# Kernel optimization log

Hardware: AMD Instinct MI355X
Metric: run time of the kernel (lower is better)

The kernel has to match this reference:

```python
import jax, jax.numpy as jnp
import numpy as np

DIM = 1024

def setup_inputs() -> dict:
    key = jax.random.key(0)
    ks = jax.random.split(key, 7)
    s = 1.0 / np.sqrt(DIM)  # roughly match nn.Linear init scale
    return {
        "x": jax.random.normal(ks[0], (4, 2048, DIM), dtype=jnp.float32),
        "Wq": jax.random.normal(ks[1], (DIM, DIM), dtype=jnp.float32) * s,
        "bq": jax.random.normal(ks[2], (DIM,), dtype=jnp.float32) * s,
        "Wk": jax.random.normal(ks[3], (DIM, DIM), dtype=jnp.float32) * s,
        "bk": jax.random.normal(ks[4], (DIM,), dtype=jnp.float32) * s,
        "Wv": jax.random.normal(ks[5], (DIM, DIM), dtype=jnp.float32) * s,
        "bv": jax.random.normal(ks[6], (DIM,), dtype=jnp.float32) * s,
    }

def reference(x, Wq, bq, Wk, bk, Wv, bv):
    # torch Linear: y = x @ W.T + b
    C = x.shape[-1]
    scale = C ** (-0.5)
    q = jnp.einsum('bnc,dc->bnd', x, Wq) + bq
    k = jnp.einsum('bnc,dc->bnd', x, Wk) + bk
    v = jnp.einsum('bnc,dc->bnd', x, Wv) + bv
    attn = jnp.einsum('bnd,bmd->bnm', q, k) * scale  # [B,N,N]
    attn = jax.nn.softmax(attn, axis=-1)
    out = jnp.einsum('bnm,bmd->bnd', attn, v)
    return out
```

## Files before the change

kernel.cpp:

```cpp
#include <hip/hip_runtime.h>

#define SEQ  2048
#define DIM  1024
#define NTOK 8192
#define NQKV 3072

typedef __attribute__((ext_vector_type(8))) __bf16 bf16x8;
typedef __attribute__((ext_vector_type(4))) float  f32x4;

__device__ __forceinline__ unsigned short f2bf(float f) {
    unsigned int u = __float_as_uint(f);
    u += 0x7fffu + ((u >> 16) & 1u);
    return (unsigned short)(u >> 16);
}

__device__ __forceinline__ float bfu2f(unsigned int lo16) {
    return __uint_as_float(lo16 << 16);
}

__device__ __forceinline__ void load_lds_128(const unsigned short* g, unsigned short* l) {
    __builtin_amdgcn_global_load_lds(
        (const __attribute__((address_space(1))) void*)g,
        (__attribute__((address_space(3))) void*)l, 16, 0, 0);
}

#define BAR() asm volatile("s_barrier" ::: "memory")

#define CLUSTER(AFR, NB, MBASE)                                            \
    do {                                                                   \
        __builtin_amdgcn_s_setprio(1);                                     \
        _Pragma("unroll")                                                  \
        for (int mf = 0; mf < 4; ++mf)                                     \
            _Pragma("unroll")                                              \
            for (int nn = 0; nn < 2; ++nn)                                 \
                _Pragma("unroll")                                          \
                for (int kk = 0; kk < 2; ++kk)                             \
                    acc[(MBASE) + mf][(NB) + nn] =                         \
                        __builtin_amdgcn_mfma_f32_16x16x32_bf16(           \
                            AFR[mf][kk], bfr[(NB) + nn][kk],               \
                            acc[(MBASE) + mf][(NB) + nn], 0, 0, 0);        \
        __builtin_amdgcn_s_setprio(0);                                     \
    } while (0)

template <int MODE, int MB>
__global__ __launch_bounds__(512, 2)
void gemm2(const unsigned short* __restrict__ A, const unsigned short* __restrict__ B,
           void* __restrict__ Cv,
           const float* __restrict__ b0v, const float* __restrict__ b1v,
           const float* __restrict__ b2v, unsigned short* __restrict__ vt,
           const float* __restrict__ inv_rs,
           int K, int lda, int ldb, int ldc,
           long sA, long sB, long sC, float alpha)
{
    constexpr int BM = MB * 128;
    constexpr int AT = BM * 64;
    constexpr int BT = 256 * 64;
    __shared__ __align__(16) unsigned short As[2 * AT];
    __shared__ __align__(16) unsigned short Bs[2 * BT];

    const int tid  = threadIdx.x;
    const int wave = tid >> 6;
    const int lane = tid & 63;
    const int l4   = lane & 15;
    const int lh   = lane >> 4;
    const int wm   = wave >> 2;
    const int wn   = wave & 3;

    const int m0 = blockIdx.x * BM;
    const int n0 = blockIdx.y * 256;
    const int z  = blockIdx.z;
    A += (long)z * sA;
    B += (long)z * sB;

    const int r0 = tid >> 3;
    const int gc = (tid & 7) ^ (r0 & 7);
    const unsigned short* Ag = A + (long)(m0 + r0) * lda + gc * 8;
    const unsigned short* Bg = B + (long)(n0 + r0) * ldb + gc * 8;
    unsigned short* Al = As + tid * 8;
    unsigned short* Bl = Bs + tid * 8;

    const int NT = K >> 6;

    auto stage = [&](int t, int u) {
        const long kof = (long)t * 64;
#pragma unroll
        for (int p = 0; p < 2 * MB; ++p)
            load_lds_128(Ag + kof + (long)(64 * p) * lda, Al + u * AT + p * 4096);
#pragma unroll
        for (int p = 0; p < 4; ++p)
            load_lds_128(Bg + kof + (long)(64 * p) * ldb, Bl + u * BT + p * 4096);
    };

    const int aoff = (wm * (BM / 2) + l4) * 64;
    const int boff = (wn * 64 + l4) * 64;
    const int cs0  = ((0 + lh) ^ (lane & 7)) * 8;
    const int cs1  = ((4 + lh) ^ (lane & 7)) * 8;

    f32x4 acc[4 * MB][4] = {};
    bf16x8 bfr[4][2], alo[4][2], ahi[4][2];

    stage(0, 0);
    asm volatile("s_waitcnt vmcnt(0)" ::: "memory");
    BAR();

    for (int t = 0; t < NT; ++t) {
        const int u = t & 1;
        const unsigned short* Ab = As + u * AT + aoff;
        const unsigned short* Bb = Bs + u * BT + boff;

#pragma unroll
        for (int nn = 0; nn < 2; ++nn) {
            bfr[nn][0] = *(const bf16x8*)(Bb + nn * 1024 + cs0);
            bfr[nn][1] = *(const bf16x8*)(Bb + nn * 1024 + cs1);
        }
#pragma unroll
        for (int mf = 0; mf < 4; ++mf) {
            alo[mf][0] = *(const bf16x8*)(Ab + mf * 1024 + cs0);
            alo[mf][1] = *(const bf16x8*)(Ab + mf * 1024 + cs1);
        }
#pragma unroll
        for (int nn = 2; nn < 4; ++nn) {
            bfr[nn][0] = *(const bf16x8*)(Bb + nn * 1024 + cs0);
            bfr[nn][1] = *(const bf16x8*)(Bb + nn * 1024 + cs1);
        }
        if (t + 1 < NT) stage(t + 1, u ^ 1);

        if constexpr (MB == 2) {
            CLUSTER(alo, 0, 0);
#pragma unroll
            for (int mf = 0; mf < 4; ++mf) {
                ahi[mf][0] = *(const bf16x8*)(Ab + (4 + mf) * 1024 + cs0);
                ahi[mf][1] = *(const bf16x8*)(Ab + (4 + mf) * 1024 + cs1);
            }
            CLUSTER(alo, 2, 0);
            CLUSTER(ahi, 2, 4);
            asm volatile("s_waitcnt vmcnt(0) lgkmcnt(0)" ::: "memory");
            BAR();
            CLUSTER(ahi, 0, 4);
        } else {
            CLUSTER(alo, 0, 0);
            asm volatile("s_waitcnt vmcnt(0) lgkmcnt(0)" ::: "memory");
            BAR();
            CLUSTER(alo, 2, 0);
        }
    }

    const int r0c = m0 + wm * (BM / 2) + lh * 4;
    const int c0c = n0 + wn * 64 + l4;

    if (MODE == 0) {
        if (n0 >= 2048) {
#pragma unroll
            for (int nf = 0; nf < 4; ++nf) {
                const int d = c0c + nf * 16 - 2048;
                const float bias = b2v[d];
#pragma unroll
                for (int mf = 0; mf < 4 * MB; ++mf) {
                    const int row = r0c + mf * 16;
                    const int bb = row >> 11;
                    const int mm = row & 2047;
                    ushort4 u;
                    u.x = f2bf(acc[mf][nf][0] + bias);
                    u.y = f2bf(acc[mf][nf][1] + bias);
                    u.z = f2bf(acc[mf][nf][2] + bias);
                    u.w = f2bf(acc[mf][nf][3] + bias);
                    *(ushort4*)(vt + ((long)bb * DIM + d) * SEQ + mm) = u;
                }
            }
        } else {
            unsigned short* C16 = (unsigned short*)Cv;
#pragma unroll
            for (int nf = 0; nf < 4; ++nf) {
                const int col = c0c + nf * 16;
                const float bias = (col >= 1024) ? b1v[col - 1024] : b0v[col];
#pragma unroll
                for (int mf = 0; mf < 4 * MB; ++mf)
#pragma unroll
                    for (int r = 0; r < 4; ++r)
                        C16[(long)(r0c + mf * 16 + r) * ldc + col] =
                            f2bf(acc[mf][nf][r] + bias);
            }
        }
    } else if (MODE == 1) {
        float* C = (float*)Cv + (long)z * sC;
        const float* ir = inv_rs + (long)z * SEQ;
#pragma unroll
        for (int mf = 0; mf < 4 * MB; ++mf) {
            const int row = r0c + mf * 16;
            const float4 inv4 = *(const float4*)(ir + row);
#pragma unroll
            for (int nf = 0; nf < 4; ++nf) {
                const int col = c0c + nf * 16;
                C[(long)(row + 0) * ldc + col] = acc[mf][nf][0] * inv4.x;
                C[(long)(row + 1) * ldc + col] = acc[mf][nf][1] * inv4.y;
                C[(long)(row + 2) * ldc + col] = acc[mf][nf][2] * inv4.z;
                C[(long)(row + 3) * ldc + col] = acc[mf][nf][3] * inv4.w;
            }
        }
    } else {
        unsigned short* C16 = (unsigned short*)Cv + (long)z * sC;
#pragma unroll
        for (int nf = 0; nf < 4; ++nf) {
            const int col = c0c + nf * 16;
#pragma unroll
            for (int mf = 0; mf < 4 * MB; ++mf)
#pragma unroll
                for (int r = 0; r < 4; ++r)
                    C16[(long)(r0c + mf * 16 + r) * ldc + col] =
                        f2bf(__expf(acc[mf][nf][r] * alpha));
        }
    }
}

__global__ __launch_bounds__(256)
void cvt_x(const float* __restrict__ src, unsigned short* __restrict__ dst, int n4)
{
    int i = blockIdx.x * 256 + threadIdx.x;
    if (i < n4) {
        float4 f = ((const float4*)src)[i];
        ushort4 u;
        u.x = f2bf(f.x); u.y = f2bf(f.y); u.z = f2bf(f.z); u.w = f2bf(f.w);
        ((ushort4*)dst)[i] = u;
    }
}

__global__ __launch_bounds__(256)
void cvt_w3(const float* __restrict__ Wq, const float* __restrict__ Wk,
            const float* __restrict__ Wv, unsigned short* __restrict__ dst)
{
    const int sel = blockIdx.y;
    const float* src = (sel == 0) ? Wq : ((sel == 1) ? Wk : Wv);
    const int i = blockIdx.x * 256 + threadIdx.x;
    float4 f = ((const float4*)src)[i];
    ushort4 u;
    u.x = f2bf(f.x); u.y = f2bf(f.y); u.z = f2bf(f.z); u.w = f2bf(f.w);
    ((ushort4*)(dst + (long)sel * DIM * DIM))[i] = u;
}

__global__ __launch_bounds__(256)
void rowsum_inv(const unsigned short* __restrict__ P, float* __restrict__ inv_rs)
{
    const int row  = blockIdx.x * 4 + (threadIdx.x >> 6);
    const int lane = threadIdx.x & 63;
    const unsigned short* pr = P + (long)row * SEQ;

    float s = 0.f;
#pragma unroll
    for (int it = 0; it < 4; ++it) {
        uint4 u = *(const uint4*)(pr + (it * 64 + lane) * 8);
        s += bfu2f(u.x & 0xffffu) + __uint_as_float(u.x & 0xffff0000u);
        s += bfu2f(u.y & 0xffffu) + __uint_as_float(u.y & 0xffff0000u);
        s += bfu2f(u.z & 0xffffu) + __uint_as_float(u.z & 0xffff0000u);
        s += bfu2f(u.w & 0xffffu) + __uint_as_float(u.w & 0xffff0000u);
    }
    for (int off = 32; off > 0; off >>= 1)
        s += __shfl_xor(s, off);
    if (lane == 0) inv_rs[row] = 1.0f / s;
}

extern "C" void kernel_launch(void* const* d_in, const int* in_sizes, int n_in,
                              void* d_out, int out_size, void* d_ws, size_t ws_size,
                              hipStream_t stream)
{
    const float* x  = (const float*)d_in[0];
    const float* Wq = (const float*)d_in[1];
    const float* bq = (const float*)d_in[2];
    const float* Wk = (const float*)d_in[3];
    const float* bk = (const float*)d_in[4];
    const float* Wv = (const float*)d_in[5];
    const float* bv = (const float*)d_in[6];
    float* out = (float*)d_out;

    char* ws = (char*)d_ws;
    unsigned short* xb   = (unsigned short*)ws;
    unsigned short* Wb   = (unsigned short*)(ws + 16u * 1024 * 1024);
    unsigned short* qkv  = (unsigned short*)(ws + 64u * 1024 * 1024);
    unsigned short* vt   = (unsigned short*)(ws + 112u * 1024 * 1024);
    unsigned short* P    = (unsigned short*)(ws + 128u * 1024 * 1024);
    float*          irs  = (float*)(ws + 160u * 1024 * 1024);

    const float scale = 0.03125f;
    dim3 blk(256);
    dim3 blk512(512);

    cvt_x<<<NTOK * DIM / 4 / 256, blk, 0, stream>>>(x, xb, NTOK * DIM / 4);
    cvt_w3<<<dim3(DIM * DIM / 4 / 256, 3), blk, 0, stream>>>(Wq, Wk, Wv, Wb);

    gemm2<0, 1><<<dim3(NTOK / 128, NQKV / 256), blk512, 0, stream>>>(
        xb, Wb, qkv, bq, bk, bv, vt, nullptr,
        DIM, DIM, DIM, NQKV, 0, 0, 0, 1.0f);

    gemm2<2, 2><<<dim3(SEQ / 256, SEQ / 256, 4), blk512, 0, stream>>>(
        qkv, qkv + 1024, P, nullptr, nullptr, nullptr, nullptr, nullptr,
        DIM, NQKV, NQKV, SEQ,
        (long)SEQ * NQKV, (long)SEQ * NQKV, (long)SEQ * SEQ, scale);

    rowsum_inv<<<NTOK / 4, blk, 0, stream>>>(P, irs);

    gemm2<1, 1><<<dim3(SEQ / 128, DIM / 256, 4), blk512, 0, stream>>>(
        P, vt, out, nullptr, nullptr, nullptr, nullptr, irs,
        SEQ, SEQ, SEQ, DIM,
        (long)SEQ * SEQ, (long)DIM * SEQ, (long)SEQ * DIM, 1.0f);
}
```

Measured before the change: 252.1 us.

## Split GEMM into QK and MN kernels with finer-grained staged LDS pipelining

Replaces the templated gemm2 with two kernels. gemm_qk keeps a 256x256 tile but splits each K-step into four quadrant phases, interleaving half-tile global-to-LDS prefetches with MFMA clusters under partial vmcnt waits. gemm_mn uses 256x128 tiles with a two-phase schedule for the QKV projection and the PV product. The intent is to overlap global loads, LDS reads and MFMA issue more tightly, at the cost of more barriers per K-step and a new tile shape for the projection and output GEMMs.

```diff
diff --git a/kernel.cpp b/kernel.cpp
--- a/kernel.cpp
+++ b/kernel.cpp
@@ -24,36 +24,36 @@
         (__attribute__((address_space(3))) void*)l, 16, 0, 0);
 }
 
-#define BAR() asm volatile("s_barrier" ::: "memory")
-
-#define CLUSTER(AFR, NB, MBASE)                                            \
+#define BAR()   asm volatile("s_barrier" ::: "memory")
+#define LGKM0() do { asm volatile("s_waitcnt lgkmcnt(0)" ::: "memory"); \
+                     __builtin_amdgcn_sched_barrier(0); } while (0)
+#define VMCNT(pf, N)                                                       \
+    do { if (pf) asm volatile("s_waitcnt vmcnt(" #N ")" ::: "memory");     \
+         else    asm volatile("s_waitcnt vmcnt(0)" ::: "memory"); } while (0)
+
+
+#define CLUS_QK(MH, NH)                                                    \
     do {                                                                   \
         __builtin_amdgcn_s_setprio(1);                                     \
         _Pragma("unroll")                                                  \
-        for (int mf = 0; mf < 4; ++mf)                                     \
+        for (int m = 0; m < 4; ++m)                                        \
             _Pragma("unroll")                                              \
-            for (int nn = 0; nn < 2; ++nn)                                 \
-                _Pragma("unroll")                                          \
-                for (int kk = 0; kk < 2; ++kk)                             \
-                    acc[(MBASE) + mf][(NB) + nn] =                         \
-                        __builtin_amdgcn_mfma_f32_16x16x32_bf16(           \
-                            AFR[mf][kk], bfr[(NB) + nn][kk],               \
-                            acc[(MBASE) + mf][(NB) + nn], 0, 0, 0);        \
+            for (int n = 0; n < 2; ++n) {                                  \
+                acc[MH][m][NH][n] = __builtin_amdgcn_mfma_f32_16x16x32_bf16( \
+                    aR[m][0], bR[n][0], acc[MH][m][NH][n], 0, 0, 0);       \
+                acc[MH][m][NH][n] = __builtin_amdgcn_mfma_f32_16x16x32_bf16( \
+                    aR[m][1], bR[n][1], acc[MH][m][NH][n], 0, 0, 0);       \
+            }                                                              \
         __builtin_amdgcn_s_setprio(0);                                     \
     } while (0)
 
-template <int MODE, int MB>
 __global__ __launch_bounds__(512, 2)
-void gemm2(const unsigned short* __restrict__ A, const unsigned short* __restrict__ B,
-           void* __restrict__ Cv,
-           const float* __restrict__ b0v, const float* __restrict__ b1v,
-           const float* __restrict__ b2v, unsigned short* __restrict__ vt,
-           const float* __restrict__ inv_rs,
-           int K, int lda, int ldb, int ldc,
-           long sA, long sB, long sC, float alpha)
-{
-    constexpr int BM = MB * 128;
-    constexpr int AT = BM * 64;
+void gemm_qk(const unsigned short* __restrict__ A, const unsigned short* __restrict__ B,
+             unsigned short* __restrict__ C,
+             int K, int lda, int ldb, int ldc,
+             long sA, long sB, long sC, float alpha)
+{
+    constexpr int AT = 256 * 64;
     constexpr int BT = 256 * 64;
     __shared__ __align__(16) unsigned short As[2 * AT];
     __shared__ __align__(16) unsigned short Bs[2 * BT];
@@ -66,7 +66,7 @@
     const int wm   = wave >> 2;
     const int wn   = wave & 3;
 
-    const int m0 = blockIdx.x * BM;
+    const int m0 = blockIdx.x * 256;
     const int n0 = blockIdx.y * 256;
     const int z  = blockIdx.z;
     A += (long)z * sA;
@@ -81,134 +81,261 @@
 
     const int NT = K >> 6;
 
-    auto stage = [&](int t, int u) {
+    auto stA = [&](int t, int u, int half) {
         const long kof = (long)t * 64;
-#pragma unroll
-        for (int p = 0; p < 2 * MB; ++p)
-            load_lds_128(Ag + kof + (long)(64 * p) * lda, Al + u * AT + p * 4096);
-#pragma unroll
-        for (int p = 0; p < 4; ++p)
-            load_lds_128(Bg + kof + (long)(64 * p) * ldb, Bl + u * BT + p * 4096);
-    };
-
-    const int aoff = (wm * (BM / 2) + l4) * 64;
-    const int boff = (wn * 64 + l4) * 64;
-    const int cs0  = ((0 + lh) ^ (lane & 7)) * 8;
+        load_lds_128(Ag + kof + (long)(64 * (2 * half + 0)) * lda, Al + u * AT + (2 * half + 0) * 4096);
+        load_lds_128(Ag + kof + (long)(64 * (2 * half + 1)) * lda, Al + u * AT + (2 * half + 1) * 4096);
+    };
+    auto stB = [&](int t, int u, int half) {
+        const long kof = (long)t * 64;
+        load_lds_128(Bg + kof + (long)(64 * (2 * half + 0)) * ldb, Bl + u * BT + (2 * half + 0) * 4096);
+        load_lds_128(Bg + kof + (long)(64 * (2 * half + 1)) * ldb, Bl + u * BT + (2 * half + 1) * 4096);
+    };
+
+    const int aoff = (wm * 64 + l4) * 64;
+    const int boff = (wn * 32 + l4) * 64;
+    const int cs0  = (lh ^ (lane & 7)) * 8;
     const int cs1  = ((4 + lh) ^ (lane & 7)) * 8;
 
-    f32x4 acc[4 * MB][4] = {};
-    bf16x8 bfr[4][2], alo[4][2], ahi[4][2];
-
-    stage(0, 0);
-    asm volatile("s_waitcnt vmcnt(0)" ::: "memory");
+    f32x4 acc[2][4][2][2] = {};
+    bf16x8 aR[4][2], bR[2][2];
+
+    auto rdA = [&](const unsigned short* Ab, int mh) {
+#pragma unroll
+        for (int m = 0; m < 4; ++m) {
+            aR[m][0] = *(const bf16x8*)(Ab + mh * 8192 + m * 1024 + cs0);
+            aR[m][1] = *(const bf16x8*)(Ab + mh * 8192 + m * 1024 + cs1);
+        }
+    };
+    auto rdB = [&](const unsigned short* Bb, int nh) {
+#pragma unroll
+        for (int n = 0; n < 2; ++n) {
+            bR[n][0] = *(const bf16x8*)(Bb + nh * 8192 + n * 1024 + cs0);
+            bR[n][1] = *(const bf16x8*)(Bb + nh * 8192 + n * 1024 + cs1);
+        }
+    };
+
+    stA(0, 0, 0); stB(0, 0, 0); stB(0, 0, 1); stA(0, 0, 1);
+    asm volatile("s_waitcnt vmcnt(4)" ::: "memory");
     BAR();
 
     for (int t = 0; t < NT; ++t) {
-        const int u = t & 1;
+        const int u  = t & 1;
+        const int pf = (t + 1 < NT);
         const unsigned short* Ab = As + u * AT + aoff;
         const unsigned short* Bb = Bs + u * BT + boff;
 
-#pragma unroll
-        for (int nn = 0; nn < 2; ++nn) {
-            bfr[nn][0] = *(const bf16x8*)(Bb + nn * 1024 + cs0);
-            bfr[nn][1] = *(const bf16x8*)(Bb + nn * 1024 + cs1);
-        }
-#pragma unroll
-        for (int mf = 0; mf < 4; ++mf) {
-            alo[mf][0] = *(const bf16x8*)(Ab + mf * 1024 + cs0);
-            alo[mf][1] = *(const bf16x8*)(Ab + mf * 1024 + cs1);
-        }
-#pragma unroll
-        for (int nn = 2; nn < 4; ++nn) {
-            bfr[nn][0] = *(const bf16x8*)(Bb + nn * 1024 + cs0);
-            bfr[nn][1] = *(const bf16x8*)(Bb + nn * 1024 + cs1);
-        }
-        if (t + 1 < NT) stage(t + 1, u ^ 1);
-
-        if constexpr (MB == 2) {
-            CLUSTER(alo, 0, 0);
-#pragma unroll
-            for (int mf = 0; mf < 4; ++mf) {
-                ahi[mf][0] = *(const bf16x8*)(Ab + (4 + mf) * 1024 + cs0);
-                ahi[mf][1] = *(const bf16x8*)(Ab + (4 + mf) * 1024 + cs1);
-            }
-            CLUSTER(alo, 2, 0);
-            CLUSTER(ahi, 2, 4);
-            asm volatile("s_waitcnt vmcnt(0) lgkmcnt(0)" ::: "memory");
-            BAR();
-            CLUSTER(ahi, 0, 4);
-        } else {
-            CLUSTER(alo, 0, 0);
-            asm volatile("s_waitcnt vmcnt(0) lgkmcnt(0)" ::: "memory");
-            BAR();
-            CLUSTER(alo, 2, 0);
-        }
+        rdA(Ab, 0); rdB(Bb, 0);
+        if (pf) stA(t + 1, u ^ 1, 0);
+        BAR(); LGKM0();
+        CLUS_QK(0, 0);
+        VMCNT(pf, 4); BAR();
+
+        rdB(Bb, 1);
+        if (pf) stB(t + 1, u ^ 1, 0);
+        BAR(); LGKM0();
+        CLUS_QK(0, 1);
+        VMCNT(pf, 4); BAR();
+
+        rdA(Ab, 1);
+        if (pf) stB(t + 1, u ^ 1, 1);
+        BAR(); LGKM0();
+        CLUS_QK(1, 1);
+        VMCNT(pf, 4); BAR();
+
+        rdB(Bb, 0);
+        if (pf) stA(t + 1, u ^ 1, 1);
+        BAR(); LGKM0();
+        CLUS_QK(1, 0);
+        VMCNT(pf, 4); BAR();
     }
 
-    const int r0c = m0 + wm * (BM / 2) + lh * 4;
-    const int c0c = n0 + wn * 64 + l4;
+    unsigned short* C16 = C + (long)z * sC;
+#pragma unroll
+    for (int mh = 0; mh < 2; ++mh)
+#pragma unroll
+        for (int m = 0; m < 4; ++m) {
+            const int rowb = m0 + mh * 128 + wm * 64 + m * 16 + lh * 4;
+#pragma unroll
+            for (int nh = 0; nh < 2; ++nh)
+#pragma unroll
+                for (int n = 0; n < 2; ++n) {
+                    const int col = n0 + nh * 128 + wn * 32 + n * 16 + l4;
+#pragma unroll
+                    for (int r = 0; r < 4; ++r)
+                        C16[(long)(rowb + r) * ldc + col] =
+                            f2bf(__expf(acc[mh][m][nh][n][r] * alpha));
+                }
+        }
+}
+
+#define CLUS_MN(MH)                                                        \
+    do {                                                                   \
+        __builtin_amdgcn_s_setprio(1);                                     \
+        _Pragma("unroll")                                                  \
+        for (int m = 0; m < 2; ++m)                                        \
+            _Pragma("unroll")                                              \
+            for (int n = 0; n < 4; ++n) {                                  \
+                acc[MH][m][n] = __builtin_amdgcn_mfma_f32_16x16x32_bf16(   \
+                    aR[m][0], bR[n][0], acc[MH][m][n], 0, 0, 0);           \
+                acc[MH][m][n] = __builtin_amdgcn_mfma_f32_16x16x32_bf16(   \
+                    aR[m][1], bR[n][1], acc[MH][m][n], 0, 0, 0);           \
+            }                                                              \
+        __builtin_amdgcn_s_setprio(0);                                     \
+    } while (0)
+
+template <int MODE>
+__global__ __launch_bounds__(512, 2)
+void gemm_mn(const unsigned short* __restrict__ A, const unsigned short* __restrict__ B,
+             void* __restrict__ Cv,
+             const float* __restrict__ b0v, const float* __restrict__ b1v,
+             const float* __restrict__ b2v, unsigned short* __restrict__ vt,
+             const float* __restrict__ inv_rs,
+             int K, int lda, int ldb, int ldc,
+             long sA, long sB, long sC)
+{
+    constexpr int AT = 256 * 64;
+    constexpr int BT = 128 * 64;
+    __shared__ __align__(16) unsigned short As[2 * AT];
+    __shared__ __align__(16) unsigned short Bs[2 * BT];
+
+    const int tid  = threadIdx.x;
+    const int wave = tid >> 6;
+    const int lane = tid & 63;
+    const int l4   = lane & 15;
+    const int lh   = lane >> 4;
+    const int wm   = wave >> 1;
+    const int wn   = wave & 1;
+
+    const int m0 = blockIdx.x * 256;
+    const int n0 = blockIdx.y * 128;
+    const int z  = blockIdx.z;
+    A += (long)z * sA;
+    B += (long)z * sB;
+
+    const int r0 = tid >> 3;
+    const int gc = (tid & 7) ^ (r0 & 7);
+    const unsigned short* Ag = A + (long)(m0 + r0) * lda + gc * 8;
+    const unsigned short* Bg = B + (long)(n0 + r0) * ldb + gc * 8;
+    unsigned short* Al = As + tid * 8;
+    unsigned short* Bl = Bs + tid * 8;
+
+    const int NT = K >> 6;
+
+    auto stA = [&](int t, int u, int half) {
+        const long kof = (long)t * 64;
+        load_lds_128(Ag + kof + (long)(64 * (2 * half + 0)) * lda, Al + u * AT + (2 * half + 0) * 4096);
+        load_lds_128(Ag + kof + (long)(64 * (2 * half + 1)) * lda, Al + u * AT + (2 * half + 1) * 4096);
+    };
+    auto stB = [&](int t, int u) {
+        const long kof = (long)t * 64;
+        load_lds_128(Bg + kof,                    Bl + u * BT);
+        load_lds_128(Bg + kof + (long)64 * ldb,   Bl + u * BT + 4096);
+    };
+
+    const int aoff = (wm * 32 + l4) * 64;
+    const int boff = (wn * 64 + l4) * 64;
+    const int cs0  = (lh ^ (lane & 7)) * 8;
+    const int cs1  = ((4 + lh) ^ (lane & 7)) * 8;
+
+    f32x4 acc[2][2][4] = {};
+    bf16x8 aR[2][2], bR[4][2];
+
+    auto rdA = [&](const unsigned short* Ab, int mh) {
+#pragma unroll
+        for (int m = 0; m < 2; ++m) {
+            aR[m][0] = *(const bf16x8*)(Ab + mh * 8192 + m * 1024 + cs0);
+            aR[m][1] = *(const bf16x8*)(Ab + mh * 8192 + m * 1024 + cs1);
+        }
+    };
+    auto rdB = [&](const unsigned short* Bb) {
+#pragma unroll
+        for (int n = 0; n < 4; ++n) {
+            bR[n][0] = *(const bf16x8*)(Bb + n * 1024 + cs0);
+            bR[n][1] = *(const bf16x8*)(Bb + n * 1024 + cs1);
+        }
+    };
+
+    stA(0, 0, 0); stB(0, 0); stA(0, 0, 1);
+    asm volatile("s_waitcnt vmcnt(2)" ::: "memory");
+    BAR();
+
+    for (int t = 0; t < NT; ++t) {
+        const int u  = t & 1;
+        const int pf = (t + 1 < NT);
+        const unsigned short* Ab = As + u * AT + aoff;
+        const unsigned short* Bb = Bs + u * BT + boff;
+
+        rdA(Ab, 0); rdB(Bb);
+        if (pf) { stA(t + 1, u ^ 1, 0); stB(t + 1, u ^ 1); }
+        BAR(); LGKM0();
+        CLUS_MN(0);
+        VMCNT(pf, 4); BAR();
+
+        rdA(Ab, 1);
+        if (pf) stA(t + 1, u ^ 1, 1);
+        BAR(); LGKM0();
+        CLUS_MN(1);
+        VMCNT(pf, 2); BAR();
+    }
 
     if (MODE == 0) {
         if (n0 >= 2048) {
 #pragma unroll
-            for (int nf = 0; nf < 4; ++nf) {
-                const int d = c0c + nf * 16 - 2048;
+            for (int n = 0; n < 4; ++n) {
+                const int d = n0 + wn * 64 + n * 16 + l4 - 2048;
                 const float bias = b2v[d];
 #pragma unroll
-                for (int mf = 0; mf < 4 * MB; ++mf) {
-                    const int row = r0c + mf * 16;
-                    const int bb = row >> 11;
-                    const int mm = row & 2047;
-                    ushort4 u;
-                    u.x = f2bf(acc[mf][nf][0] + bias);
-                    u.y = f2bf(acc[mf][nf][1] + bias);
-                    u.z = f2bf(acc[mf][nf][2] + bias);
-                    u.w = f2bf(acc[mf][nf][3] + bias);
-                    *(ushort4*)(vt + ((long)bb * DIM + d) * SEQ + mm) = u;
-                }
+                for (int mh = 0; mh < 2; ++mh)
+#pragma unroll
+                    for (int m = 0; m < 2; ++m) {
+                        const int row = m0 + mh * 128 + wm * 32 + m * 16 + lh * 4;
+                        const int bb = row >> 11;
+                        const int mm = row & 2047;
+                        ushort4 uu;
+                        uu.x = f2bf(acc[mh][m][n][0] + bias);
+                        uu.y = f2bf(acc[mh][m][n][1] + bias);
+                        uu.z = f2bf(acc[mh][m][n][2] + bias);
+                        uu.w = f2bf(acc[mh][m][n][3] + bias);
+                        *(ushort4*)(vt + ((long)bb * DIM + d) * SEQ + mm) = uu;
+                    }
             }
         } else {
             unsigned short* C16 = (unsigned short*)Cv;
 #pragma unroll
-            for (int nf = 0; nf < 4; ++nf) {
-                const int col = c0c + nf * 16;
+            for (int n = 0; n < 4; ++n) {
+                const int col = n0 + wn * 64 + n * 16 + l4;
                 const float bias = (col >= 1024) ? b1v[col - 1024] : b0v[col];
 #pragma unroll
-                for (int mf = 0; mf < 4 * MB; ++mf)
-#pragma unroll
-                    for (int r = 0; r < 4; ++r)
-                        C16[(long)(r0c + mf * 16 + r) * ldc + col] =
-                            f2bf(acc[mf][nf][r] + bias);
+                for (int mh = 0; mh < 2; ++mh)
+#pragma unroll
+                    for (int m = 0; m < 2; ++m) {
+                        const int rowb = m0 + mh * 128 + wm * 32 + m * 16 + lh * 4;
+#pragma unroll
+                        for (int r = 0; r < 4; ++r)
+                            C16[(long)(rowb + r) * ldc + col] =
+                                f2bf(acc[mh][m][n][r] + bias);
+                    }
             }
         }
-    } else if (MODE == 1) {
+    } else {
         float* C = (float*)Cv + (long)z * sC;
         const float* ir = inv_rs + (long)z * SEQ;
 #pragma unroll
-        for (int mf = 0; mf < 4 * MB; ++mf) {
-            const int row = r0c + mf * 16;
-            const float4 inv4 = *(const float4*)(ir + row);
-#pragma unroll
-            for (int nf = 0; nf < 4; ++nf) {
-                const int col = c0c + nf * 16;
-                C[(long)(row + 0) * ldc + col] = acc[mf][nf][0] * inv4.x;
-                C[(long)(row + 1) * ldc + col] = acc[mf][nf][1] * inv4.y;
-                C[(long)(row + 2) * ldc + col] = acc[mf][nf][2] * inv4.z;
-                C[(long)(row + 3) * ldc + col] = acc[mf][nf][3] * inv4.w;
+        for (int mh = 0; mh < 2; ++mh)
+#pragma unroll
+            for (int m = 0; m < 2; ++m) {
+                const int rowb = m0 + mh * 128 + wm * 32 + m * 16 + lh * 4;
+                const float4 inv4 = *(const float4*)(ir + rowb);
+#pragma unroll
+                for (int n = 0; n < 4; ++n) {
+                    const int col = n0 + wn * 64 + n * 16 + l4;
+                    C[(long)(rowb + 0) * ldc + col] = acc[mh][m][n][0] * inv4.x;
+                    C[(long)(rowb + 1) * ldc + col] = acc[mh][m][n][1] * inv4.y;
+                    C[(long)(rowb + 2) * ldc + col] = acc[mh][m][n][2] * inv4.z;
+                    C[(long)(rowb + 3) * ldc + col] = acc[mh][m][n][3] * inv4.w;
+                }
             }
-        }
-    } else {
-        unsigned short* C16 = (unsigned short*)Cv + (long)z * sC;
-#pragma unroll
-        for (int nf = 0; nf < 4; ++nf) {
-            const int col = c0c + nf * 16;
-#pragma unroll
-            for (int mf = 0; mf < 4 * MB; ++mf)
-#pragma unroll
-                for (int r = 0; r < 4; ++r)
-                    C16[(long)(r0c + mf * 16 + r) * ldc + col] =
-                        f2bf(__expf(acc[mf][nf][r] * alpha));
-        }
     }
 }
 
@@ -286,19 +413,19 @@
     cvt_x<<<NTOK * DIM / 4 / 256, blk, 0, stream>>>(x, xb, NTOK * DIM / 4);
     cvt_w3<<<dim3(DIM * DIM / 4 / 256, 3), blk, 0, stream>>>(Wq, Wk, Wv, Wb);
 
-    gemm2<0, 1><<<dim3(NTOK / 128, NQKV / 256), blk512, 0, stream>>>(
+    gemm_mn<0><<<dim3(NTOK / 256, NQKV / 128), blk512, 0, stream>>>(
         xb, Wb, qkv, bq, bk, bv, vt, nullptr,
-        DIM, DIM, DIM, NQKV, 0, 0, 0, 1.0f);
-
-    gemm2<2, 2><<<dim3(SEQ / 256, SEQ / 256, 4), blk512, 0, stream>>>(
-        qkv, qkv + 1024, P, nullptr, nullptr, nullptr, nullptr, nullptr,
+        DIM, DIM, DIM, NQKV, 0, 0, 0);
+
+    gemm_qk<<<dim3(SEQ / 256, SEQ / 256, 4), blk512, 0, stream>>>(
+        qkv, qkv + 1024, P,
         DIM, NQKV, NQKV, SEQ,
         (long)SEQ * NQKV, (long)SEQ * NQKV, (long)SEQ * SEQ, scale);
 
     rowsum_inv<<<NTOK / 4, blk, 0, stream>>>(P, irs);
 
-    gemm2<1, 1><<<dim3(SEQ / 128, DIM / 256, 4), blk512, 0, stream>>>(
+    gemm_mn<1><<<dim3(SEQ / 256, DIM / 128, 4), blk512, 0, stream>>>(
         P, vt, out, nullptr, nullptr, nullptr, nullptr, irs,
         SEQ, SEQ, SEQ, DIM,
-        (long)SEQ * SEQ, (long)DIM * SEQ, (long)SEQ * DIM, 1.0f);
-}
+        (long)SEQ * SEQ, (long)DIM * SEQ, (long)SEQ * DIM);
+}
```

Result: no change. 248.5 us (-1.4%).
